# Performance work log

Measured on AMD Instinct MI355X. Metric: run time of the kernel, lower is better.

The kernel has to match this reference:

```python
import jax, jax.numpy as jnp
import numpy as np

DT_MIN = 0.001  # config.rsp_dt_min
HARMONIC_SCALE = 0.1


def phi(z):
    # ResonantActivation: SiLU plus small harmonic term (harmonic_scale=0.1)
    return jax.nn.silu(z) + HARMONIC_SCALE * jnp.sin(z)


def setup_inputs() -> dict:
    key = jax.random.key(0)
    ks = jax.random.split(key, 8)
    B, L, D = 4, 2048, 1024
    std = 1.0 / np.sqrt(D)
    inp = {
        "x": jax.random.normal(ks[0], (B, L, D), dtype=jnp.float32),
        "f_prev": jnp.zeros((B, D), dtype=jnp.float32),
        "s_prev": jnp.zeros((B, D), dtype=jnp.float32),
        "w_lambda": jnp.zeros((D,), dtype=jnp.float32),
        "P_lambda_w": jax.random.uniform(ks[1], (D, D), jnp.float32, -std, std),
        "W_beta_w": jax.random.uniform(ks[2], (D, D), jnp.float32, -std, std),
        "W_alpha_w": jax.random.uniform(ks[3], (D, D), jnp.float32, -std, std),
        "W_alpha_b": jnp.full((D,), -3.0, dtype=jnp.float32),  # rsp_init_bias_alpha
        "W_rho_w": 0.01 * jax.random.normal(ks[4], (D, 3 * D), dtype=jnp.float32),
        "W_rho_b": jnp.full((D,), 2.0, dtype=jnp.float32),  # rsp_init_bias_rho
        "out_proj_w": 0.02 * jax.random.normal(ks[5], (D, D), dtype=jnp.float32),
        "res_scale": jnp.ones((1,), dtype=jnp.float32),
    }
    return inp


def _rsp_forward(x, f_prev, s_prev, w_lambda, P_lambda_w, W_beta_w,
                 W_alpha_w, W_alpha_b, W_rho_w, W_rho_b, out_proj_w, res_scale):
    # x: [B, L, D]
    # Input-dependent decay: lambda = exp(-exp(clip(w + x @ P^T)))
    lnl = jnp.clip(w_lambda + jnp.einsum('bld,ed->ble', x, P_lambda_w), -4.0, 4.0)
    lam = jnp.clip(jnp.exp(-jnp.exp(lnl)), DT_MIN, 1.0 - DT_MIN)

    B_gate = phi(jnp.einsum('bld,ed->ble', x, W_beta_w))
    alpha = jax.nn.sigmoid(jnp.einsum('bld,ed->ble', x, W_alpha_w) + W_alpha_b)

    # inject f_prev into first step's input contribution
    b_in = B_gate.at[:, 0, :].set(lam[:, 0, :] * f_prev + B_gate[:, 0, :])

    # fast linear recurrence: h_t = lam_t * h_{t-1} + b_t   (scan over L)
    lam_t = jnp.moveaxis(lam, 1, 0)      # [L, B, D]
    b_t = jnp.moveaxis(b_in, 1, 0)       # [L, B, D]

    def fast_step(h, lb):
        l, b = lb
        h = l * h + b
        return h, h

    _, f_seq = jax.lax.scan(fast_step, jnp.zeros_like(f_prev), (lam_t, b_t))
    f_states = jnp.moveaxis(f_seq, 0, 1)  # [B, L, D]

    # slow EMA: s_t = s_{t-1} + alpha_t * (f_t - s_{t-1})
    a_t = jnp.moveaxis(alpha, 1, 0)

    def slow_step(s, af):
        a, f = af
        s = s + a * (f - s)
        return s, s

    _, s_seq = jax.lax.scan(slow_step, s_prev, (a_t, f_seq))
    s_states = jnp.moveaxis(s_seq, 0, 1)  # [B, L, D]

    gate_input = jnp.concatenate([f_states, s_states, x], axis=-1)  # [B, L, 3D]
    rho = jax.nn.sigmoid(jnp.einsum('blk,ek->ble', gate_input, W_rho_w) + W_rho_b)
    h = rho * f_states + (1.0 - rho) * s_states
    h = x + res_scale * jnp.einsum('bld,ed->ble', h, out_proj_w)
    return h, f_states[:, -1, :], s_states[:, -1, :]


def reference(x, f_prev, s_prev, w_lambda, P_lambda_w, W_beta_w, W_alpha_w,
              W_alpha_b, W_rho_w, W_rho_b, out_proj_w, res_scale):
    return _rsp_forward(x, f_prev, s_prev, w_lambda, P_lambda_w, W_beta_w,
                        W_alpha_w, W_alpha_b, W_rho_w, W_rho_b, out_proj_w, res_scale)
```

## Files before the change

### kernel.cpp

```cpp
#include <hip/hip_runtime.h>

#define Bb 4
#define Ll 2048
#define Dd 1024
#define Mm (Bb*Ll)
#define NCH 64
#define CLEN (Ll/NCH)

typedef __attribute__((ext_vector_type(4))) float f32x4;
typedef __attribute__((ext_vector_type(8))) short s16x8;
typedef __attribute__((ext_vector_type(4))) short s16x4;

__device__ __forceinline__ float sigm(float v){ return 1.0f/(1.0f+__expf(-v)); }

__device__ __forceinline__ short bf16rne(float f){
  unsigned u = __builtin_bit_cast(unsigned, f);
  u += 0x7fffu + ((u>>16)&1u);
  return (short)(u>>16);
}

__device__ __forceinline__ void gl_lds16(const void* g, void* l){
  __builtin_amdgcn_global_load_lds((__attribute__((address_space(1))) void*)g,
                                   (__attribute__((address_space(3))) void*)l, 16, 0, 0);
}

template<int EPI>
__launch_bounds__(256)
__global__ void gemm_bt(const short* __restrict__ A0, const short* __restrict__ A1,
                        const short* __restrict__ A2, const short* __restrict__ W,
                        int K,
                        const float* __restrict__ v0, const float* __restrict__ p0,
                        const float* __restrict__ p1,
                        float* __restrict__ of, short* __restrict__ oh)
{
  __shared__ short As[128*32];
  __shared__ short Bs[128*32];
  const int tid  = threadIdx.x;
  const int lane = tid & 63;
  const int wid  = tid >> 6;
  const int wm = wid >> 1, wn = wid & 1;
  const long bm0 = (long)blockIdx.x * 128;
  const long bn0 = (long)blockIdx.y * 128;

  f32x4 acc[4][4] = {};

  const int r0 = tid >> 2;
  const int r1 = (256 + tid) >> 2;
  const int sg = (tid & 3) * 8;

  for (int k0 = 0; k0 < K; k0 += 32) {
    const short* Asrc = A0; long acol = k0;
    if (EPI == 3) {
      const int blk = k0 >> 10;
      Asrc = (blk == 0) ? A0 : ((blk == 1) ? A1 : A2);
      acol = k0 & 1023;
    }
    gl_lds16(Asrc + (bm0 + r0)*1024 + acol + sg, As + tid*8);
    gl_lds16(Asrc + (bm0 + r1)*1024 + acol + sg, As + (256 + tid)*8);
    gl_lds16(W + (bn0 + r0)*(long)K + k0 + sg, Bs + tid*8);
    gl_lds16(W + (bn0 + r1)*(long)K + k0 + sg, Bs + (256 + tid)*8);
    __syncthreads();

    s16x8 af[4], bf[4];
    #pragma unroll
    for (int mi = 0; mi < 4; ++mi)
      af[mi] = *(const s16x8*)&As[(wm*64 + mi*16 + (lane & 15))*32 + (lane >> 4)*8];
    #pragma unroll
    for (int ni = 0; ni < 4; ++ni)
      bf[ni] = *(const s16x8*)&Bs[(wn*64 + ni*16 + (lane & 15))*32 + (lane >> 4)*8];

    #pragma unroll
    for (int mi = 0; mi < 4; ++mi)
      #pragma unroll
      for (int ni = 0; ni < 4; ++ni)
        asm("v_mfma_f32_16x16x32_bf16 %0, %1, %2, %0"
            : "+v"(acc[mi][ni]) : "v"(af[mi]), "v"(bf[ni]));
    __syncthreads();
  }

  const float rs = (EPI == 4) ? p1[0] : 0.0f;
  const int ecol0 = (int)bn0 + wn*64 + (lane & 15);
  const int erow0 = (int)bm0 + wm*64 + ((lane >> 4) << 2);

  #pragma unroll
  for (int mi = 0; mi < 4; ++mi) {
    #pragma unroll
    for (int ni = 0; ni < 4; ++ni) {
      asm volatile("s_nop 7\n\ts_nop 7\n\ts_nop 7" : "+v"(acc[mi][ni]));
      const f32x4 v = acc[mi][ni];
      const int gn = ecol0 + ni*16;
      #pragma unroll
      for (int j = 0; j < 4; ++j) {
        const long gm  = erow0 + mi*16 + j;
        const long idx = gm*1024 + gn;
        const float val = v[j];
        if (EPI == 0) {
          float z = val + v0[gn];
          z = fminf(fmaxf(z, -4.0f), 4.0f);
          float l = __expf(-__expf(z));
          of[idx] = fminf(fmaxf(l, 0.001f), 0.999f);
        } else if (EPI == 1) {
          of[idx] = val*sigm(val) + 0.1f*__sinf(val);
        } else if (EPI == 2) {
          of[idx] = sigm(val + v0[gn]);
        } else if (EPI == 3) {
          const float r = sigm(val + v0[gn]);
          const float h = r*p0[idx] + (1.0f - r)*p1[idx];
          oh[idx] = bf16rne(h);
        } else {
          of[idx] = p0[idx] + rs*val;
        }
      }
    }
  }
}


__global__ void f_chunk1(const float* __restrict__ lm, const float* __restrict__ bgp,
                         const float* __restrict__ fprev,
                         float* __restrict__ cP, float* __restrict__ cB)
{
  const int d = blockIdx.x*256 + threadIdx.x;
  const int c = blockIdx.y, b = blockIdx.z;
  float P = 1.0f, Bv = 0.0f;
  size_t base = ((size_t)b*Ll + (size_t)c*CLEN)*Dd + d;
  const float fp = (c == 0) ? fprev[b*Dd + d] : 0.0f;
  for (int t = 0; t < CLEN; ++t) {
    const float l = lm[base];
    float bb = bgp[base];
    if (c == 0 && t == 0) bb += l*fp;
    P *= l;
    Bv = l*Bv + bb;
    base += Dd;
  }
  const size_t ci = ((size_t)b*NCH + c)*Dd + d;
  cP[ci] = P; cB[ci] = Bv;
}

__global__ void scan_carry(const float* __restrict__ cP, const float* __restrict__ cB,
                           const float* __restrict__ init,
                           float* __restrict__ H0, float* __restrict__ last_out)
{
  const int d = blockIdx.x*256 + threadIdx.x;
  const int b = blockIdx.y;
  float h = init ? init[b*Dd + d] : 0.0f;
  for (int c = 0; c < NCH; ++c) {
    const size_t ci = ((size_t)b*NCH + c)*Dd + d;
    H0[ci] = h;
    h = cP[ci]*h + cB[ci];
  }
  last_out[b*Dd + d] = h;
}

__global__ void f_chunk3(const float* __restrict__ lm, const float* __restrict__ bgp,
                         const float* __restrict__ fprev, const float* __restrict__ H0,
                         float* __restrict__ fo, short* __restrict__ fob)
{
  const int d = blockIdx.x*256 + threadIdx.x;
  const int c = blockIdx.y, b = blockIdx.z;
  float h = H0[((size_t)b*NCH + c)*Dd + d];
  size_t base = ((size_t)b*Ll + (size_t)c*CLEN)*Dd + d;
  const float fp = (c == 0) ? fprev[b*Dd + d] : 0.0f;
  for (int t = 0; t < CLEN; ++t) {
    const float l = lm[base];
    float bb = bgp[base];
    if (c == 0 && t == 0) bb += l*fp;
    h = l*h + bb;
    fo[base] = h;
    fob[base] = bf16rne(h);
    base += Dd;
  }
}

__global__ void s_chunk1(const float* __restrict__ alp, const float* __restrict__ fst,
                         float* __restrict__ cP, float* __restrict__ cB)
{
  const int d = blockIdx.x*256 + threadIdx.x;
  const int c = blockIdx.y, b = blockIdx.z;
  float P = 1.0f, Bv = 0.0f;
  size_t base = ((size_t)b*Ll + (size_t)c*CLEN)*Dd + d;
  for (int t = 0; t < CLEN; ++t) {
    const float a = alp[base];
    const float l = 1.0f - a;
    P *= l;
    Bv = l*Bv + a*fst[base];
    base += Dd;
  }
  const size_t ci = ((size_t)b*NCH + c)*Dd + d;
  cP[ci] = P; cB[ci] = Bv;
}

__global__ void s_chunk3(const float* __restrict__ alp, const float* __restrict__ fst,
                         const float* __restrict__ H0,
                         float* __restrict__ so, short* __restrict__ sob)
{
  const int d = blockIdx.x*256 + threadIdx.x;
  const int c = blockIdx.y, b = blockIdx.z;
  float h = H0[((size_t)b*NCH + c)*Dd + d];
  size_t base = ((size_t)b*Ll + (size_t)c*CLEN)*Dd + d;
  for (int t = 0; t < CLEN; ++t) {
    const float a = alp[base];
    h = h + a*(fst[base] - h);
    so[base] = h;
    sob[base] = bf16rne(h);
    base += Dd;
  }
}

__global__ void cvt_bf16(const float* __restrict__ src, short* __restrict__ dst, int n4)
{
  int i = blockIdx.x*256 + threadIdx.x;
  const int stride = gridDim.x*256;
  for (; i < n4; i += stride) {
    const f32x4 v = ((const f32x4*)src)[i];
    s16x4 o;
    o[0] = bf16rne(v[0]); o[1] = bf16rne(v[1]);
    o[2] = bf16rne(v[2]); o[3] = bf16rne(v[3]);
    ((s16x4*)dst)[i] = o;
  }
}

extern "C" void kernel_launch(void* const* d_in, const int* in_sizes, int n_in,
                              void* d_out, int out_size, void* d_ws, size_t ws_size,
                              hipStream_t stream)
{
  (void)in_sizes; (void)n_in; (void)out_size; (void)ws_size;
  const float* x   = (const float*)d_in[0];
  const float* fpv = (const float*)d_in[1];
  const float* spv = (const float*)d_in[2];
  const float* wl  = (const float*)d_in[3];
  const float* Pw  = (const float*)d_in[4];
  const float* Wbw = (const float*)d_in[5];
  const float* Waw = (const float*)d_in[6];
  const float* ab  = (const float*)d_in[7];
  const float* Wr  = (const float*)d_in[8];
  const float* rb  = (const float*)d_in[9];
  const float* Wo  = (const float*)d_in[10];
  const float* rs  = (const float*)d_in[11];

  float* out    = (float*)d_out;
  float* f_last = out + (size_t)Mm*Dd;
  float* s_last = f_last + (size_t)Bb*Dd;

  char* w = (char*)d_ws;
  auto alloc = [&](size_t bytes){ char* p = w; w += (bytes + 255) & ~(size_t)255; return p; };
  short* xb   = (short*)alloc((size_t)Mm*Dd*2);
  short* pb   = (short*)alloc((size_t)Dd*Dd*2);
  short* wbb  = (short*)alloc((size_t)Dd*Dd*2);
  short* wab  = (short*)alloc((size_t)Dd*Dd*2);
  short* wrb  = (short*)alloc((size_t)Dd*3*Dd*2);
  short* opb  = (short*)alloc((size_t)Dd*Dd*2);
  float* lam  = (float*)alloc((size_t)Mm*Dd*4);
  float* bg   = (float*)alloc((size_t)Mm*Dd*4);
  float* al   = (float*)alloc((size_t)Mm*Dd*4);
  float* f32f = (float*)alloc((size_t)Mm*Dd*4);
  float* s32  = (float*)alloc((size_t)Mm*Dd*4);
  short* fb   = (short*)alloc((size_t)Mm*Dd*2);
  short* sb   = (short*)alloc((size_t)Mm*Dd*2);
  float* cP   = (float*)alloc((size_t)Bb*NCH*Dd*4);
  float* cB   = (float*)alloc((size_t)Bb*NCH*Dd*4);
  float* H0   = (float*)alloc((size_t)Bb*NCH*Dd*4);
  short* hm   = (short*)lam;

  auto cvt = [&](const float* s_, short* d_, size_t n){
    int n4 = (int)(n/4);
    int grid = (n4 + 255)/256; if (grid > 2048) grid = 2048;
    cvt_bf16<<<dim3(grid), dim3(256), 0, stream>>>(s_, d_, n4);
  };
  cvt(x,   xb,  (size_t)Mm*Dd);
  cvt(Pw,  pb,  (size_t)Dd*Dd);
  cvt(Wbw, wbb, (size_t)Dd*Dd);
  cvt(Waw, wab, (size_t)Dd*Dd);
  cvt(Wr,  wrb, (size_t)Dd*3*Dd);
  cvt(Wo,  opb, (size_t)Dd*Dd);

  const dim3 gg(Mm/128, Dd/128);
  gemm_bt<0><<<gg, dim3(256), 0, stream>>>(xb, nullptr, nullptr, pb,  Dd,   wl, nullptr, nullptr, lam, nullptr);
  gemm_bt<1><<<gg, dim3(256), 0, stream>>>(xb, nullptr, nullptr, wbb, Dd,   nullptr, nullptr, nullptr, bg, nullptr);
  gemm_bt<2><<<gg, dim3(256), 0, stream>>>(xb, nullptr, nullptr, wab, Dd,   ab, nullptr, nullptr, al, nullptr);

  const dim3 gs(Dd/256, NCH, Bb);
  const dim3 gc(Dd/256, Bb);
  f_chunk1<<<gs, dim3(256), 0, stream>>>(lam, bg, fpv, cP, cB);
  scan_carry<<<gc, dim3(256), 0, stream>>>(cP, cB, (const float*)nullptr, H0, f_last);
  f_chunk3<<<gs, dim3(256), 0, stream>>>(lam, bg, fpv, H0, f32f, fb);

  s_chunk1<<<gs, dim3(256), 0, stream>>>(al, f32f, cP, cB);
  scan_carry<<<gc, dim3(256), 0, stream>>>(cP, cB, spv, H0, s_last);
  s_chunk3<<<gs, dim3(256), 0, stream>>>(al, f32f, H0, s32, sb);

  gemm_bt<3><<<gg, dim3(256), 0, stream>>>(fb, sb, xb, wrb, 3*Dd, rb, f32f, s32, nullptr, hm);
  gemm_bt<4><<<gg, dim3(256), 0, stream>>>(hm, nullptr, nullptr, opb, Dd, nullptr, x, rs, out, nullptr);
}
```

Before: 413.2 us.

## Fuse input GEMMs, double-buffer LDS, store intermediates in bf16, fuse f-scan with s-chunk pass

Merges the three input projections into one GEMM over a concatenated weight matrix, with a per-segment epilogue. Adds double-buffered LDS staging to the GEMM loop and swaps the grid axes so blocks sharing a row tile launch together. Stores B_gate, alpha, f and s as bf16 instead of fp32 and fuses the f-chunk pass with the s-chunk reduction, removing a kernel and several fp32 round trips. This cuts memory traffic at the cost of extra precision loss in the recurrences: the slow scan now runs on bf16-rounded f and alpha.

```diff
diff --git a/kernel.cpp b/kernel.cpp
--- a/kernel.cpp
+++ b/kernel.cpp
@@ -18,6 +18,10 @@
   u += 0x7fffu + ((u>>16)&1u);
   return (short)(u>>16);
 }
+__device__ __forceinline__ float bf2f(short s){
+  unsigned u = ((unsigned)(unsigned short)s) << 16;
+  return __builtin_bit_cast(float, u);
+}
 
 __device__ __forceinline__ void gl_lds16(const void* g, void* l){
   __builtin_amdgcn_global_load_lds((__attribute__((address_space(1))) void*)g,
@@ -29,18 +33,20 @@
 __global__ void gemm_bt(const short* __restrict__ A0, const short* __restrict__ A1,
                         const short* __restrict__ A2, const short* __restrict__ W,
                         int K,
-                        const float* __restrict__ v0, const float* __restrict__ p0,
-                        const float* __restrict__ p1,
-                        float* __restrict__ of, short* __restrict__ oh)
-{
-  __shared__ short As[128*32];
-  __shared__ short Bs[128*32];
+                        const float* __restrict__ b0, const float* __restrict__ b1,
+                        const float* __restrict__ xres, const float* __restrict__ rsp,
+                        const short* __restrict__ fB, const short* __restrict__ sB,
+                        float* __restrict__ oF, short* __restrict__ oB0,
+                        short* __restrict__ oB1)
+{
+  __shared__ short As[2][128*32];
+  __shared__ short Bs[2][128*32];
   const int tid  = threadIdx.x;
   const int lane = tid & 63;
   const int wid  = tid >> 6;
   const int wm = wid >> 1, wn = wid & 1;
-  const long bm0 = (long)blockIdx.x * 128;
-  const long bn0 = (long)blockIdx.y * 128;
+  const long bn0 = (long)blockIdx.x * 128;
+  const long bm0 = (long)blockIdx.y * 128;
 
   f32x4 acc[4][4] = {};
 
@@ -48,37 +54,48 @@
   const int r1 = (256 + tid) >> 2;
   const int sg = (tid & 3) * 8;
 
-  for (int k0 = 0; k0 < K; k0 += 32) {
+  auto stage = [&](int buf, int k0){
     const short* Asrc = A0; long acol = k0;
     if (EPI == 3) {
       const int blk = k0 >> 10;
       Asrc = (blk == 0) ? A0 : ((blk == 1) ? A1 : A2);
       acol = k0 & 1023;
     }
-    gl_lds16(Asrc + (bm0 + r0)*1024 + acol + sg, As + tid*8);
-    gl_lds16(Asrc + (bm0 + r1)*1024 + acol + sg, As + (256 + tid)*8);
-    gl_lds16(W + (bn0 + r0)*(long)K + k0 + sg, Bs + tid*8);
-    gl_lds16(W + (bn0 + r1)*(long)K + k0 + sg, Bs + (256 + tid)*8);
-    __syncthreads();
-
-    s16x8 af[4], bf[4];
+    gl_lds16(Asrc + (bm0 + r0)*1024 + acol + sg, &As[buf][(size_t)tid*8]);
+    gl_lds16(Asrc + (bm0 + r1)*1024 + acol + sg, &As[buf][(size_t)(256+tid)*8]);
+    gl_lds16(W + (bn0 + r0)*(long)K + k0 + sg, &Bs[buf][(size_t)tid*8]);
+    gl_lds16(W + (bn0 + r1)*(long)K + k0 + sg, &Bs[buf][(size_t)(256+tid)*8]);
+  };
+
+  auto compute = [&](int buf){
+    s16x8 af[4], bfr[4];
     #pragma unroll
     for (int mi = 0; mi < 4; ++mi)
-      af[mi] = *(const s16x8*)&As[(wm*64 + mi*16 + (lane & 15))*32 + (lane >> 4)*8];
+      af[mi] = *(const s16x8*)&As[buf][(wm*64 + mi*16 + (lane & 15))*32 + (lane >> 4)*8];
     #pragma unroll
     for (int ni = 0; ni < 4; ++ni)
-      bf[ni] = *(const s16x8*)&Bs[(wn*64 + ni*16 + (lane & 15))*32 + (lane >> 4)*8];
-
+      bfr[ni] = *(const s16x8*)&Bs[buf][(wn*64 + ni*16 + (lane & 15))*32 + (lane >> 4)*8];
     #pragma unroll
     for (int mi = 0; mi < 4; ++mi)
       #pragma unroll
       for (int ni = 0; ni < 4; ++ni)
         asm("v_mfma_f32_16x16x32_bf16 %0, %1, %2, %0"
-            : "+v"(acc[mi][ni]) : "v"(af[mi]), "v"(bf[ni]));
+            : "+v"(acc[mi][ni]) : "v"(af[mi]), "v"(bfr[ni]));
+  };
+
+  stage(0, 0);
+  __syncthreads();
+  int cur = 0;
+  for (int k0 = 32; k0 < K; k0 += 32) {
+    stage(cur ^ 1, k0);
+    compute(cur);
     __syncthreads();
-  }
-
-  const float rs = (EPI == 4) ? p1[0] : 0.0f;
+    cur ^= 1;
+  }
+  compute(cur);
+
+  const float rs = (EPI == 4) ? rsp[0] : 0.0f;
+  const int seg = (EPI == 5) ? (int)(bn0 >> 10) : 0;
   const int ecol0 = (int)bn0 + wn*64 + (lane & 15);
   const int erow0 = (int)bm0 + wm*64 + ((lane >> 4) << 2);
 
@@ -89,26 +106,30 @@
       asm volatile("s_nop 7\n\ts_nop 7\n\ts_nop 7" : "+v"(acc[mi][ni]));
       const f32x4 v = acc[mi][ni];
       const int gn = ecol0 + ni*16;
+      const int cn = gn & 1023;
       #pragma unroll
       for (int j = 0; j < 4; ++j) {
         const long gm  = erow0 + mi*16 + j;
-        const long idx = gm*1024 + gn;
+        const long idx = gm*1024 + cn;
         const float val = v[j];
-        if (EPI == 0) {
-          float z = val + v0[gn];
-          z = fminf(fmaxf(z, -4.0f), 4.0f);
-          float l = __expf(-__expf(z));
-          of[idx] = fminf(fmaxf(l, 0.001f), 0.999f);
-        } else if (EPI == 1) {
-          of[idx] = val*sigm(val) + 0.1f*__sinf(val);
-        } else if (EPI == 2) {
-          of[idx] = sigm(val + v0[gn]);
+        if (EPI == 5) {
+          if (seg == 0) {
+            float z = val + b0[cn];
+            z = fminf(fmaxf(z, -4.0f), 4.0f);
+            float l = __expf(-__expf(z));
+            oF[idx] = fminf(fmaxf(l, 0.001f), 0.999f);
+          } else if (seg == 1) {
+            oB0[idx] = bf16rne(val*sigm(val) + 0.1f*__sinf(val));
+          } else {
+            oB1[idx] = bf16rne(sigm(val + b1[cn]));
+          }
         } else if (EPI == 3) {
-          const float r = sigm(val + v0[gn]);
-          const float h = r*p0[idx] + (1.0f - r)*p1[idx];
-          oh[idx] = bf16rne(h);
+          const float r = sigm(val + b0[cn]);
+          const float f = bf2f(fB[idx]);
+          const float s = bf2f(sB[idx]);
+          oB0[idx] = bf16rne(r*f + (1.0f - r)*s);
         } else {
-          of[idx] = p0[idx] + rs*val;
+          oF[idx] = xres[idx] + rs*val;
         }
       }
     }
@@ -116,7 +137,7 @@
 }
 
 
-__global__ void f_chunk1(const float* __restrict__ lm, const float* __restrict__ bgp,
+__global__ void f_chunk1(const float* __restrict__ lm, const short* __restrict__ bgB,
                          const float* __restrict__ fprev,
                          float* __restrict__ cP, float* __restrict__ cB)
 {
@@ -127,7 +148,7 @@
   const float fp = (c == 0) ? fprev[b*Dd + d] : 0.0f;
   for (int t = 0; t < CLEN; ++t) {
     const float l = lm[base];
-    float bb = bgp[base];
+    float bb = bf2f(bgB[base]);
     if (c == 0 && t == 0) bb += l*fp;
     P *= l;
     Bv = l*Bv + bb;
@@ -152,56 +173,47 @@
   last_out[b*Dd + d] = h;
 }
 
-__global__ void f_chunk3(const float* __restrict__ lm, const float* __restrict__ bgp,
-                         const float* __restrict__ fprev, const float* __restrict__ H0,
-                         float* __restrict__ fo, short* __restrict__ fob)
+__global__ void fs_mid(const float* __restrict__ lm, const short* __restrict__ bgB,
+                       const float* __restrict__ fprev, const float* __restrict__ H0f,
+                       const short* __restrict__ alB,
+                       short* __restrict__ fob, float* __restrict__ cPs,
+                       float* __restrict__ cBs)
 {
   const int d = blockIdx.x*256 + threadIdx.x;
   const int c = blockIdx.y, b = blockIdx.z;
-  float h = H0[((size_t)b*NCH + c)*Dd + d];
+  float h = H0f[((size_t)b*NCH + c)*Dd + d];
+  float sP = 1.0f, sBv = 0.0f;
   size_t base = ((size_t)b*Ll + (size_t)c*CLEN)*Dd + d;
   const float fp = (c == 0) ? fprev[b*Dd + d] : 0.0f;
   for (int t = 0; t < CLEN; ++t) {
     const float l = lm[base];
-    float bb = bgp[base];
+    float bb = bf2f(bgB[base]);
     if (c == 0 && t == 0) bb += l*fp;
     h = l*h + bb;
-    fo[base] = h;
-    fob[base] = bf16rne(h);
+    const short hr = bf16rne(h);
+    fob[base] = hr;
+    const float fr = bf2f(hr);
+    const float a = bf2f(alB[base]);
+    sP *= (1.0f - a);
+    sBv = (1.0f - a)*sBv + a*fr;
     base += Dd;
   }
-}
-
-__global__ void s_chunk1(const float* __restrict__ alp, const float* __restrict__ fst,
-                         float* __restrict__ cP, float* __restrict__ cB)
+  const size_t ci = ((size_t)b*NCH + c)*Dd + d;
+  cPs[ci] = sP; cBs[ci] = sBv;
+}
+
+__global__ void s_chunk3(const float* __restrict__ alB_unused_f32, const short* __restrict__ alB,
+                         const short* __restrict__ fob, const float* __restrict__ H0s,
+                         short* __restrict__ sob)
 {
   const int d = blockIdx.x*256 + threadIdx.x;
   const int c = blockIdx.y, b = blockIdx.z;
-  float P = 1.0f, Bv = 0.0f;
+  float h = H0s[((size_t)b*NCH + c)*Dd + d];
   size_t base = ((size_t)b*Ll + (size_t)c*CLEN)*Dd + d;
   for (int t = 0; t < CLEN; ++t) {
-    const float a = alp[base];
-    const float l = 1.0f - a;
-    P *= l;
-    Bv = l*Bv + a*fst[base];
-    base += Dd;
-  }
-  const size_t ci = ((size_t)b*NCH + c)*Dd + d;
-  cP[ci] = P; cB[ci] = Bv;
-}
-
-__global__ void s_chunk3(const float* __restrict__ alp, const float* __restrict__ fst,
-                         const float* __restrict__ H0,
-                         float* __restrict__ so, short* __restrict__ sob)
-{
-  const int d = blockIdx.x*256 + threadIdx.x;
-  const int c = blockIdx.y, b = blockIdx.z;
-  float h = H0[((size_t)b*NCH + c)*Dd + d];
-  size_t base = ((size_t)b*Ll + (size_t)c*CLEN)*Dd + d;
-  for (int t = 0; t < CLEN; ++t) {
-    const float a = alp[base];
-    h = h + a*(fst[base] - h);
-    so[base] = h;
+    const float a = bf2f(alB[base]);
+    const float f = bf2f(fob[base]);
+    h = h + a*(f - h);
     sob[base] = bf16rne(h);
     base += Dd;
   }
@@ -245,16 +257,12 @@
   char* w = (char*)d_ws;
   auto alloc = [&](size_t bytes){ char* p = w; w += (bytes + 255) & ~(size_t)255; return p; };
   short* xb   = (short*)alloc((size_t)Mm*Dd*2);
-  short* pb   = (short*)alloc((size_t)Dd*Dd*2);
-  short* wbb  = (short*)alloc((size_t)Dd*Dd*2);
-  short* wab  = (short*)alloc((size_t)Dd*Dd*2);
+  short* w3   = (short*)alloc((size_t)3*Dd*Dd*2);
   short* wrb  = (short*)alloc((size_t)Dd*3*Dd*2);
   short* opb  = (short*)alloc((size_t)Dd*Dd*2);
   float* lam  = (float*)alloc((size_t)Mm*Dd*4);
-  float* bg   = (float*)alloc((size_t)Mm*Dd*4);
-  float* al   = (float*)alloc((size_t)Mm*Dd*4);
-  float* f32f = (float*)alloc((size_t)Mm*Dd*4);
-  float* s32  = (float*)alloc((size_t)Mm*Dd*4);
+  short* bgB  = (short*)alloc((size_t)Mm*Dd*2);
+  short* alB  = (short*)alloc((size_t)Mm*Dd*2);
   short* fb   = (short*)alloc((size_t)Mm*Dd*2);
   short* sb   = (short*)alloc((size_t)Mm*Dd*2);
   float* cP   = (float*)alloc((size_t)Bb*NCH*Dd*4);
@@ -267,28 +275,30 @@
     int grid = (n4 + 255)/256; if (grid > 2048) grid = 2048;
     cvt_bf16<<<dim3(grid), dim3(256), 0, stream>>>(s_, d_, n4);
   };
-  cvt(x,   xb,  (size_t)Mm*Dd);
-  cvt(Pw,  pb,  (size_t)Dd*Dd);
-  cvt(Wbw, wbb, (size_t)Dd*Dd);
-  cvt(Waw, wab, (size_t)Dd*Dd);
-  cvt(Wr,  wrb, (size_t)Dd*3*Dd);
-  cvt(Wo,  opb, (size_t)Dd*Dd);
-
-  const dim3 gg(Mm/128, Dd/128);
-  gemm_bt<0><<<gg, dim3(256), 0, stream>>>(xb, nullptr, nullptr, pb,  Dd,   wl, nullptr, nullptr, lam, nullptr);
-  gemm_bt<1><<<gg, dim3(256), 0, stream>>>(xb, nullptr, nullptr, wbb, Dd,   nullptr, nullptr, nullptr, bg, nullptr);
-  gemm_bt<2><<<gg, dim3(256), 0, stream>>>(xb, nullptr, nullptr, wab, Dd,   ab, nullptr, nullptr, al, nullptr);
+  cvt(x,   xb,            (size_t)Mm*Dd);
+  cvt(Pw,  w3,            (size_t)Dd*Dd);
+  cvt(Wbw, w3 +   Dd*Dd,  (size_t)Dd*Dd);
+  cvt(Waw, w3 + 2*Dd*Dd,  (size_t)Dd*Dd);
+  cvt(Wr,  wrb,           (size_t)Dd*3*Dd);
+  cvt(Wo,  opb,           (size_t)Dd*Dd);
+
+  gemm_bt<5><<<dim3(3*Dd/128, Mm/128), dim3(256), 0, stream>>>(
+      xb, nullptr, nullptr, w3, Dd, wl, ab, nullptr, nullptr, nullptr, nullptr,
+      lam, bgB, alB);
 
   const dim3 gs(Dd/256, NCH, Bb);
   const dim3 gc(Dd/256, Bb);
-  f_chunk1<<<gs, dim3(256), 0, stream>>>(lam, bg, fpv, cP, cB);
+  f_chunk1<<<gs, dim3(256), 0, stream>>>(lam, bgB, fpv, cP, cB);
   scan_carry<<<gc, dim3(256), 0, stream>>>(cP, cB, (const float*)nullptr, H0, f_last);
-  f_chunk3<<<gs, dim3(256), 0, stream>>>(lam, bg, fpv, H0, f32f, fb);
-
-  s_chunk1<<<gs, dim3(256), 0, stream>>>(al, f32f, cP, cB);
+  fs_mid<<<gs, dim3(256), 0, stream>>>(lam, bgB, fpv, H0, alB, fb, cP, cB);
   scan_carry<<<gc, dim3(256), 0, stream>>>(cP, cB, spv, H0, s_last);
-  s_chunk3<<<gs, dim3(256), 0, stream>>>(al, f32f, H0, s32, sb);
-
-  gemm_bt<3><<<gg, dim3(256), 0, stream>>>(fb, sb, xb, wrb, 3*Dd, rb, f32f, s32, nullptr, hm);
-  gemm_bt<4><<<gg, dim3(256), 0, stream>>>(hm, nullptr, nullptr, opb, Dd, nullptr, x, rs, out, nullptr);
-}
+  s_chunk3<<<gs, dim3(256), 0, stream>>>(nullptr, alB, fb, H0, sb);
+
+  gemm_bt<3><<<dim3(Dd/128, Mm/128), dim3(256), 0, stream>>>(
+      fb, sb, xb, wrb, 3*Dd, rb, nullptr, nullptr, nullptr, fb, sb,
+      nullptr, hm, nullptr);
+
+  gemm_bt<4><<<dim3(Dd/128, Mm/128), dim3(256), 0, stream>>>(
+      hm, nullptr, nullptr, opb, Dd, nullptr, nullptr, x, rs, nullptr, nullptr,
+      out, nullptr, nullptr);
+}
```

Result: faster. 389.9 us (-5.6%).
